# Kernel tuning notes

Measured on AMD Instinct MI355X. Metric: run time of the kernel, lower is better.

The kernel has to match this reference:

```python
import jax, jax.numpy as jnp
import numpy as np

NV = 6890          # SMPL vertex count
NF = 13776         # SMPL face count
N_CHUNKS = 10
EUCL_THRES = 0.02  # euclthres
WN_THRES = 0.99    # exterior if winding number <= 0.99


def _winding_numbers(points, tris):
    """Generalized winding numbers of `points` [m,3] w.r.t. triangle soup `tris` [f,3,3].
    Solid angle per (point, triangle) via the van-Oosterom/Strackee atan2 formula."""
    r = tris[None, :, :, :] - points[:, None, None, :]   # [m,f,3,3]
    ra, rb, rc = r[:, :, 0, :], r[:, :, 1, :], r[:, :, 2, :]
    la = jnp.linalg.norm(ra, axis=-1)
    lb = jnp.linalg.norm(rb, axis=-1)
    lc = jnp.linalg.norm(rc, axis=-1)
    det = jnp.einsum('mfi,mfi->mf', ra, jnp.cross(rb, rc))
    denom = (la * lb * lc
             + jnp.sum(ra * rb, -1) * lc
             + jnp.sum(rb * rc, -1) * la
             + jnp.sum(rc * ra, -1) * lb)
    omega = 2.0 * jnp.arctan2(det, denom)                # [m,f]
    return jnp.sum(omega, axis=-1) / (4.0 * jnp.pi)      # [m]


def setup_inputs() -> dict:
    key = jax.random.key(0)
    k1, k2, k3 = jax.random.split(key, 3)
    vertices = jax.random.normal(k1, (1, NV, 3), dtype=jnp.float32)
    faces = jax.random.randint(k2, (NF, 3), 0, NV)
    # geodesic-distance >= geothres mask: symmetric, False on the diagonal
    gm = jax.random.uniform(k3, (NV, NV)) > 0.3
    gm = gm & gm.T
    gm = gm.at[jnp.arange(NV), jnp.arange(NV)].set(False)
    return {"vertices": vertices, "faces": faces, "geomask": gm}


def reference(vertices, faces, geomask):
    # triangles(vertices): gather face corner coordinates  [NF,3,3] (bs=1)
    tris = vertices[0][faces]
    # get_intersection_mask: chunked winding numbers, exterior = wn <= 0.99
    pts = vertices[0].reshape(N_CHUNKS, NV // N_CHUNKS, 3)
    wn = jax.lax.map(lambda p: _winding_numbers(p, tris), pts).reshape(NV)
    exterior = (wn <= WN_THRES)[None, :]                 # [1,NV] bool
    # batch_pairwise_dist (squared=False)
    x = vertices[0]                                      # [NV,3]
    sq = jnp.sum(x * x, axis=-1)
    d2 = sq[:, None] + sq[None, :] - 2.0 * (x @ x.T)
    v2v = jnp.sqrt(jnp.maximum(d2, 0.0))                 # [NV,NV]
    # mask geodesically-near pairs with inf, take per-vertex min over dim 1
    masked = jnp.where(geomask, v2v, jnp.inf)
    idx = jnp.argmin(masked, axis=0)                     # argmin over rows for each column
    v2v_min = v2v[jnp.arange(NV), idx][None, :]          # gather along dim 2 (symmetric)
    incontact = v2v_min < EUCL_THRES
    return v2v_min, incontact, exterior
```

## Files before the change

kernel.cpp:

```cpp
#include <hip/hip_runtime.h>
#include <hip/hip_bf16.h>
#include <math.h>

#define NV 6890
#define NF 13776
#define NVPAD 6912
#define NPBLK 27
#define TCH 64
#define TPC 216
#define WN_THRES 0.99
#define EUCL_THRES 0.02f

#define WS_TRIS_OFF   64
#define WS_X4_OFF     (64 + NF*48)
#define WS_PART_OFF   (64 + NF*48 + NV*16)

__global__ __launch_bounds__(256) void prep_kernel(
    const float* __restrict__ verts, const int* __restrict__ faces,
    const unsigned char* __restrict__ gm_bytes,
    float* __restrict__ tris12, float* __restrict__ x4, int* __restrict__ flag)
{
    int t = blockIdx.x * 256 + threadIdx.x;

    if (t < NF) {
        int ia = faces[t*3+0], ib = faces[t*3+1], ic = faces[t*3+2];
        float* o = tris12 + (size_t)t * 12;
        o[0]  = verts[ia*3+0]; o[1]  = verts[ia*3+1]; o[2]  = verts[ia*3+2]; o[3]  = 0.f;
        o[4]  = verts[ib*3+0]; o[5]  = verts[ib*3+1]; o[6]  = verts[ib*3+2]; o[7]  = 0.f;
        o[8]  = verts[ic*3+0]; o[9]  = verts[ic*3+1]; o[10] = verts[ic*3+2]; o[11] = 0.f;
    }
    if (t < NV) {
        float x = verts[t*3+0], y = verts[t*3+1], z = verts[t*3+2];
        x4[t*4+0] = x; x4[t*4+1] = y; x4[t*4+2] = z;
        x4[t*4+3] = (x*x + y*y) + z*z;
    }
    if (blockIdx.x == 0 && threadIdx.x < 64) {
        int lane = threadIdx.x;
        bool any3F = false, anyNZmod = false;
        for (int k = 0; k < 64; ++k) {
            int off = lane * 64 + k;
            unsigned char b = gm_bytes[off];
            if ((off & 3) == 3 && (b == 0x3F || b == 0xBF)) any3F = true;
            if ((off & 3) != 0 && b != 0) anyNZmod = true;
        }
        unsigned long long m3F = __ballot(any3F);
        unsigned long long mNZ = __ballot(anyNZmod);
        if (lane == 0) {
            *flag = m3F ? 2 : (mNZ ? 0 : 1);
        }
    }
}

__device__ __forceinline__ float fast_atan2f(float y, float x)
{
    float ay = __builtin_fabsf(y), ax = __builtin_fabsf(x);
    float mx = fmaxf(ax, ay);
    float mn = fminf(ax, ay);
    float r  = __builtin_amdgcn_rcpf(fmaxf(mx, 1e-37f));
    float t  = mn * r;
    float s  = t * t;
    float u  =              0.00282363896258175373077393f;
    u = fmaf(u, s, -0.0159569028764963150024414f);
    u = fmaf(u, s,  0.0425049886107444763183594f);
    u = fmaf(u, s, -0.0748900920152664184570312f);
    u = fmaf(u, s,  0.106347933411598205566406f);
    u = fmaf(u, s, -0.142027363181114196777344f);
    u = fmaf(u, s,  0.199926957488059997558594f);
    u = fmaf(u, s, -0.333331018686294555664062f);
    float p = fmaf(s * u, t, t);
    p = (ay > ax)  ? (1.5707963267948966f - p) : p;
    p = (x < 0.0f) ? (3.14159265358979323846f - p) : p;
    return copysignf(p, y);
}

__global__ __launch_bounds__(256) void wn_kernel(
    const float4* __restrict__ tris12, const float4* __restrict__ x4,
    float* __restrict__ partials)
{
    int pt = blockIdx.x * 256 + threadIdx.x;
    int tc = blockIdx.y;
    int t0 = tc * TPC;
    int nt = min(TPC, NF - t0);

    float4 P = x4[min(pt, NV - 1)];
    float px = P.x, py = P.y, pz = P.z;

    const float4* __restrict__ T = tris12 + (size_t)t0 * 3;

    double acc = 0.0;
    #pragma unroll 2
    for (int k = 0; k < nt; ++k) {
        float4 A = T[3*k+0];
        float4 B = T[3*k+1];
        float4 C = T[3*k+2];
        float ax = A.x - px, ay = A.y - py, az = A.z - pz;
        float bx = B.x - px, by = B.y - py, bz = B.z - pz;
        float cx = C.x - px, cy = C.y - py, cz = C.z - pz;

        float la = __builtin_amdgcn_sqrtf((ax*ax + ay*ay) + az*az);
        float lb = __builtin_amdgcn_sqrtf((bx*bx + by*by) + bz*bz);
        float lc = __builtin_amdgcn_sqrtf((cx*cx + cy*cy) + cz*cz);

        float ux = by*cz - bz*cy;
        float uy = bz*cx - bx*cz;
        float uz = bx*cy - by*cx;
        float det = (ax*ux + ay*uy) + az*uz;

        float dab = (ax*bx + ay*by) + az*bz;
        float dbc = (bx*cx + by*cy) + bz*cz;
        float dca = (cx*ax + cy*ay) + cz*az;

        float denom = la*lb*lc + dab*lc + dbc*la + dca*lb;

        acc += (double)fast_atan2f(det, denom);
    }

    partials[(size_t)tc * NVPAD + pt] = (float)acc;
}

__global__ __launch_bounds__(256) void wn_reduce_kernel(
    const float* __restrict__ partials, float* __restrict__ out_exterior)
{
    int pt = blockIdx.x * 256 + threadIdx.x;
    if (pt >= NV) return;
    double s = 0.0;
    for (int t = 0; t < TCH; ++t) s += (double)partials[(size_t)t * NVPAD + pt];
    double wn = (2.0 * s) / 12.566370614359172953850573533118;
    out_exterior[pt] = (wn <= WN_THRES) ? 1.0f : 0.0f;
}

__device__ __forceinline__ void acc_min(float& m, const float4* __restrict__ x4,
                                        int i, bool g,
                                        float xj, float yj, float zj, float sqj)
{
    float4 vi = x4[i];
    float dot = (vi.x*xj + vi.y*yj) + vi.z*zj;
    float d2  = vi.w + sqj - 2.0f * dot;
    m = fminf(m, g ? d2 : INFINITY);
}

__global__ __launch_bounds__(256) void v2v_kernel(
    const void* __restrict__ gm, const float4* __restrict__ x4,
    const int* __restrict__ flag_p, float* __restrict__ out)
{
    int j = blockIdx.x;
    int tid = threadIdx.x;
    int flag = *flag_p;

    float4 vj = x4[j];
    float xj = vj.x, yj = vj.y, zj = vj.z, sqj = vj.w;

    float m = INFINITY;

    if (flag == 0) {
        const unsigned char* row = (const unsigned char*)gm + (size_t)j * NV;
        int lead = (int)((4u - ((uintptr_t)row & 3u)) & 3u);
        int nw = (NV - lead) >> 2;
        int base = lead + nw * 4;
        int ntail = NV - base;
        if (tid < lead) acc_min(m, x4, tid, row[tid] != 0, xj, yj, zj, sqj);
        const unsigned int* wrow = (const unsigned int*)(row + lead);
        for (int w = tid; w < nw; w += 256) {
            unsigned int v = wrow[w];
            int i0 = lead + w * 4;
            acc_min(m, x4, i0+0, (v & 0x000000FFu) != 0, xj, yj, zj, sqj);
            acc_min(m, x4, i0+1, (v & 0x0000FF00u) != 0, xj, yj, zj, sqj);
            acc_min(m, x4, i0+2, (v & 0x00FF0000u) != 0, xj, yj, zj, sqj);
            acc_min(m, x4, i0+3, (v & 0xFF000000u) != 0, xj, yj, zj, sqj);
        }
        if (tid < ntail) acc_min(m, x4, base + tid, row[base + tid] != 0, xj, yj, zj, sqj);
    } else if (flag == 1) {
        const uint2* row = (const uint2*)((const int*)gm + (size_t)j * NV);
        for (int w = tid; w < NV/2; w += 256) {
            uint2 v = row[w];
            int i0 = w * 2;
            acc_min(m, x4, i0+0, v.x != 0, xj, yj, zj, sqj);
            acc_min(m, x4, i0+1, v.y != 0, xj, yj, zj, sqj);
        }
    } else {
        const float2* row = (const float2*)((const float*)gm + (size_t)j * NV);
        for (int w = tid; w < NV/2; w += 256) {
            float2 v = row[w];
            int i0 = w * 2;
            acc_min(m, x4, i0+0, v.x != 0.0f, xj, yj, zj, sqj);
            acc_min(m, x4, i0+1, v.y != 0.0f, xj, yj, zj, sqj);
        }
    }

    __shared__ float red[256];
    red[tid] = m;
    __syncthreads();
    for (int s = 128; s > 0; s >>= 1) {
        if (tid < s) red[tid] = fminf(red[tid], red[tid + s]);
        __syncthreads();
    }
    if (tid == 0) {
        float d = __builtin_amdgcn_sqrtf(fmaxf(red[0], 0.f));
        out[j] = d;
        out[NV + j] = (d < EUCL_THRES) ? 1.f : 0.f;
    }
}

extern "C" void kernel_launch(void* const* d_in, const int* in_sizes, int n_in,
                              void* d_out, int out_size, void* d_ws, size_t ws_size,
                              hipStream_t stream)
{
    const float* verts = (const float*)d_in[0];
    const int*   faces = (const int*)d_in[1];
    const void*  gm    = d_in[2];
    float* out = (float*)d_out;
    char* ws = (char*)d_ws;

    int*   flag     = (int*)ws;
    float* tris12   = (float*)(ws + WS_TRIS_OFF);
    float* x4       = (float*)(ws + WS_X4_OFF);
    float* partials = (float*)(ws + WS_PART_OFF);

    int nprep = (NF > NV ? NF : NV);
    prep_kernel<<<(nprep + 255) / 256, 256, 0, stream>>>(
        verts, faces, (const unsigned char*)gm, tris12, x4, flag);

    wn_kernel<<<dim3(NPBLK, TCH), 256, 0, stream>>>(
        (const float4*)tris12, (const float4*)x4, partials);

    wn_reduce_kernel<<<NPBLK, 256, 0, stream>>>(partials, out + 2 * NV);

    v2v_kernel<<<NV, 256, 0, stream>>>(gm, (const float4*)x4, flag, out);
}
```

Baseline: 520.9 us.

## Fuse v2v and winding-number kernels into one launch with wave-per-row v2v

Merges the pairwise-distance min kernel and the winding-number kernel into a single launch, with blocks split by index between the two jobs so both run concurrently. The v2v path now gives each 64-lane wave one row and reduces with shuffles instead of a shared-memory tree with block barriers. The triangle and point buffers are padded with zeros so the winding loop runs a fixed trip count with 4-way unrolling, and each group of four atan2 results is summed in float before being added to the double accumulator. Risks include byte-wise gm loads that are no longer vectorized, a slight precision change from float partial sums, and load imbalance between the two block types.

New measurement: 501.9 us. 3.7% less time.

```diff
diff --git a/kernel.cpp b/kernel.cpp
--- a/kernel.cpp
+++ b/kernel.cpp
@@ -1,19 +1,21 @@
 #include <hip/hip_runtime.h>
-#include <hip/hip_bf16.h>
 #include <math.h>
 
 #define NV 6890
 #define NF 13776
 #define NVPAD 6912
+#define NFPAD 13824
 #define NPBLK 27
 #define TCH 64
 #define TPC 216
+#define V2V_BLOCKS 1723
+#define WN_BLOCKS (NPBLK*TCH)
 #define WN_THRES 0.99
 #define EUCL_THRES 0.02f
 
 #define WS_TRIS_OFF   64
-#define WS_X4_OFF     (64 + NF*48)
-#define WS_PART_OFF   (64 + NF*48 + NV*16)
+#define WS_X4_OFF     (64 + NFPAD*48)
+#define WS_PART_OFF   (WS_X4_OFF + NVPAD*16)
 
 __global__ __launch_bounds__(256) void prep_kernel(
     const float* __restrict__ verts, const int* __restrict__ faces,
@@ -22,17 +24,26 @@
 {
     int t = blockIdx.x * 256 + threadIdx.x;
 
-    if (t < NF) {
-        int ia = faces[t*3+0], ib = faces[t*3+1], ic = faces[t*3+2];
+    if (t < NFPAD) {
         float* o = tris12 + (size_t)t * 12;
-        o[0]  = verts[ia*3+0]; o[1]  = verts[ia*3+1]; o[2]  = verts[ia*3+2]; o[3]  = 0.f;
-        o[4]  = verts[ib*3+0]; o[5]  = verts[ib*3+1]; o[6]  = verts[ib*3+2]; o[7]  = 0.f;
-        o[8]  = verts[ic*3+0]; o[9]  = verts[ic*3+1]; o[10] = verts[ic*3+2]; o[11] = 0.f;
-    }
-    if (t < NV) {
-        float x = verts[t*3+0], y = verts[t*3+1], z = verts[t*3+2];
-        x4[t*4+0] = x; x4[t*4+1] = y; x4[t*4+2] = z;
-        x4[t*4+3] = (x*x + y*y) + z*z;
+        if (t < NF) {
+            int ia = faces[t*3+0], ib = faces[t*3+1], ic = faces[t*3+2];
+            o[0]  = verts[ia*3+0]; o[1]  = verts[ia*3+1]; o[2]  = verts[ia*3+2]; o[3]  = 0.f;
+            o[4]  = verts[ib*3+0]; o[5]  = verts[ib*3+1]; o[6]  = verts[ib*3+2]; o[7]  = 0.f;
+            o[8]  = verts[ic*3+0]; o[9]  = verts[ic*3+1]; o[10] = verts[ic*3+2]; o[11] = 0.f;
+        } else {
+            #pragma unroll
+            for (int q = 0; q < 12; ++q) o[q] = 0.f;
+        }
+    }
+    if (t < NVPAD) {
+        if (t < NV) {
+            float x = verts[t*3+0], y = verts[t*3+1], z = verts[t*3+2];
+            x4[t*4+0] = x; x4[t*4+1] = y; x4[t*4+2] = z;
+            x4[t*4+3] = (x*x + y*y) + z*z;
+        } else {
+            x4[t*4+0] = 0.f; x4[t*4+1] = 0.f; x4[t*4+2] = 0.f; x4[t*4+3] = 0.f;
+        }
     }
     if (blockIdx.x == 0 && threadIdx.x < 64) {
         int lane = threadIdx.x;
@@ -73,49 +84,108 @@
     return copysignf(p, y);
 }
 
-__global__ __launch_bounds__(256) void wn_kernel(
+__global__ __launch_bounds__(256) void fused_kernel(
     const float4* __restrict__ tris12, const float4* __restrict__ x4,
-    float* __restrict__ partials)
-{
-    int pt = blockIdx.x * 256 + threadIdx.x;
-    int tc = blockIdx.y;
-    int t0 = tc * TPC;
-    int nt = min(TPC, NF - t0);
-
-    float4 P = x4[min(pt, NV - 1)];
-    float px = P.x, py = P.y, pz = P.z;
-
-    const float4* __restrict__ T = tris12 + (size_t)t0 * 3;
-
-    double acc = 0.0;
-    #pragma unroll 2
-    for (int k = 0; k < nt; ++k) {
-        float4 A = T[3*k+0];
-        float4 B = T[3*k+1];
-        float4 C = T[3*k+2];
-        float ax = A.x - px, ay = A.y - py, az = A.z - pz;
-        float bx = B.x - px, by = B.y - py, bz = B.z - pz;
-        float cx = C.x - px, cy = C.y - py, cz = C.z - pz;
-
-        float la = __builtin_amdgcn_sqrtf((ax*ax + ay*ay) + az*az);
-        float lb = __builtin_amdgcn_sqrtf((bx*bx + by*by) + bz*bz);
-        float lc = __builtin_amdgcn_sqrtf((cx*cx + cy*cy) + cz*cz);
-
-        float ux = by*cz - bz*cy;
-        float uy = bz*cx - bx*cz;
-        float uz = bx*cy - by*cx;
-        float det = (ax*ux + ay*uy) + az*uz;
-
-        float dab = (ax*bx + ay*by) + az*bz;
-        float dbc = (bx*cx + by*cy) + bz*cz;
-        float dca = (cx*ax + cy*ay) + cz*az;
-
-        float denom = la*lb*lc + dab*lc + dbc*la + dca*lb;
-
-        acc += (double)fast_atan2f(det, denom);
-    }
-
-    partials[(size_t)tc * NVPAD + pt] = (float)acc;
+    float* __restrict__ partials,
+    const void* __restrict__ gm, const int* __restrict__ flag_p,
+    float* __restrict__ out)
+{
+    if (blockIdx.x < V2V_BLOCKS) {
+        int w = threadIdx.x >> 6;
+        int lane = threadIdx.x & 63;
+        int j = blockIdx.x * 4 + w;
+        if (j >= NV) return;
+
+        int flag = *flag_p;
+        float4 vj = x4[j];
+        float m = INFINITY;
+
+#define V2V_BODY(GTEST)                                            \
+        {                                                          \
+            int i0 = 0;                                            \
+            for (; i0 + 64 <= NV; i0 += 64) {                      \
+                int i = i0 + lane;                                 \
+                bool g = (GTEST);                                  \
+                float4 vi = x4[i];                                 \
+                float dot = (vi.x*vj.x + vi.y*vj.y) + vi.z*vj.z;   \
+                float d2  = vi.w + vj.w - 2.0f*dot;                \
+                m = fminf(m, g ? d2 : INFINITY);                   \
+            }                                                      \
+            int i = i0 + lane;                                     \
+            if (i < NV) {                                          \
+                bool g = (GTEST);                                  \
+                float4 vi = x4[i];                                 \
+                float dot = (vi.x*vj.x + vi.y*vj.y) + vi.z*vj.z;   \
+                float d2  = vi.w + vj.w - 2.0f*dot;                \
+                m = fminf(m, g ? d2 : INFINITY);                   \
+            }                                                      \
+        }
+
+        if (flag == 0) {
+            const unsigned char* row = (const unsigned char*)gm + (size_t)j * NV;
+            V2V_BODY(row[i] != 0)
+        } else if (flag == 1) {
+            const int* row = (const int*)gm + (size_t)j * NV;
+            V2V_BODY(row[i] != 0)
+        } else {
+            const float* row = (const float*)gm + (size_t)j * NV;
+            V2V_BODY(row[i] != 0.0f)
+        }
+#undef V2V_BODY
+
+        #pragma unroll
+        for (int k = 32; k > 0; k >>= 1)
+            m = fminf(m, __shfl_xor(m, k, 64));
+        if (lane == 0) {
+            float d = __builtin_amdgcn_sqrtf(fmaxf(m, 0.f));
+            out[j] = d;
+            out[NV + j] = (d < EUCL_THRES) ? 1.f : 0.f;
+        }
+    } else {
+        int wnb = blockIdx.x - V2V_BLOCKS;
+        int tc = wnb / NPBLK;
+        int pb = wnb - tc * NPBLK;
+        int pt = pb * 256 + threadIdx.x;
+
+        float4 P = x4[pt];
+        float px = P.x, py = P.y, pz = P.z;
+        const float4* __restrict__ T = tris12 + (size_t)tc * (TPC * 3);
+
+        double acc = 0.0;
+        for (int kk = 0; kk < TPC; kk += 4) {
+            float s4 = 0.f;
+            #pragma unroll
+            for (int u = 0; u < 4; ++u) {
+                const float4* Tk = T + 3 * (kk + u);
+                float4 A = Tk[0];
+                float4 B = Tk[1];
+                float4 C = Tk[2];
+                float ax = A.x - px, ay = A.y - py, az = A.z - pz;
+                float bx = B.x - px, by = B.y - py, bz = B.z - pz;
+                float cx = C.x - px, cy = C.y - py, cz = C.z - pz;
+
+                float la = __builtin_amdgcn_sqrtf((ax*ax + ay*ay) + az*az);
+                float lb = __builtin_amdgcn_sqrtf((bx*bx + by*by) + bz*bz);
+                float lc = __builtin_amdgcn_sqrtf((cx*cx + cy*cy) + cz*cz);
+
+                float ux = by*cz - bz*cy;
+                float uy = bz*cx - bx*cz;
+                float uz = bx*cy - by*cx;
+                float det = (ax*ux + ay*uy) + az*uz;
+
+                float dab = (ax*bx + ay*by) + az*bz;
+                float dbc = (bx*cx + by*cy) + bz*cz;
+                float dca = (cx*ax + cy*ay) + cz*az;
+
+                float denom = la*lb*lc + dab*lc + dbc*la + dca*lb;
+
+                s4 += fast_atan2f(det, denom);
+            }
+            acc += (double)s4;
+        }
+
+        partials[(size_t)tc * NVPAD + pt] = (float)acc;
+    }
 }
 
 __global__ __launch_bounds__(256) void wn_reduce_kernel(
@@ -129,78 +199,6 @@
     out_exterior[pt] = (wn <= WN_THRES) ? 1.0f : 0.0f;
 }
 
-__device__ __forceinline__ void acc_min(float& m, const float4* __restrict__ x4,
-                                        int i, bool g,
-                                        float xj, float yj, float zj, float sqj)
-{
-    float4 vi = x4[i];
-    float dot = (vi.x*xj + vi.y*yj) + vi.z*zj;
-    float d2  = vi.w + sqj - 2.0f * dot;
-    m = fminf(m, g ? d2 : INFINITY);
-}
-
-__global__ __launch_bounds__(256) void v2v_kernel(
-    const void* __restrict__ gm, const float4* __restrict__ x4,
-    const int* __restrict__ flag_p, float* __restrict__ out)
-{
-    int j = blockIdx.x;
-    int tid = threadIdx.x;
-    int flag = *flag_p;
-
-    float4 vj = x4[j];
-    float xj = vj.x, yj = vj.y, zj = vj.z, sqj = vj.w;
-
-    float m = INFINITY;
-
-    if (flag == 0) {
-        const unsigned char* row = (const unsigned char*)gm + (size_t)j * NV;
-        int lead = (int)((4u - ((uintptr_t)row & 3u)) & 3u);
-        int nw = (NV - lead) >> 2;
-        int base = lead + nw * 4;
-        int ntail = NV - base;
-        if (tid < lead) acc_min(m, x4, tid, row[tid] != 0, xj, yj, zj, sqj);
-        const unsigned int* wrow = (const unsigned int*)(row + lead);
-        for (int w = tid; w < nw; w += 256) {
-            unsigned int v = wrow[w];
-            int i0 = lead + w * 4;
-            acc_min(m, x4, i0+0, (v & 0x000000FFu) != 0, xj, yj, zj, sqj);
-            acc_min(m, x4, i0+1, (v & 0x0000FF00u) != 0, xj, yj, zj, sqj);
-            acc_min(m, x4, i0+2, (v & 0x00FF0000u) != 0, xj, yj, zj, sqj);
-            acc_min(m, x4, i0+3, (v & 0xFF000000u) != 0, xj, yj, zj, sqj);
-        }
-        if (tid < ntail) acc_min(m, x4, base + tid, row[base + tid] != 0, xj, yj, zj, sqj);
-    } else if (flag == 1) {
-        const uint2* row = (const uint2*)((const int*)gm + (size_t)j * NV);
-        for (int w = tid; w < NV/2; w += 256) {
-            uint2 v = row[w];
-            int i0 = w * 2;
-            acc_min(m, x4, i0+0, v.x != 0, xj, yj, zj, sqj);
-            acc_min(m, x4, i0+1, v.y != 0, xj, yj, zj, sqj);
-        }
-    } else {
-        const float2* row = (const float2*)((const float*)gm + (size_t)j * NV);
-        for (int w = tid; w < NV/2; w += 256) {
-            float2 v = row[w];
-            int i0 = w * 2;
-            acc_min(m, x4, i0+0, v.x != 0.0f, xj, yj, zj, sqj);
-            acc_min(m, x4, i0+1, v.y != 0.0f, xj, yj, zj, sqj);
-        }
-    }
-
-    __shared__ float red[256];
-    red[tid] = m;
-    __syncthreads();
-    for (int s = 128; s > 0; s >>= 1) {
-        if (tid < s) red[tid] = fminf(red[tid], red[tid + s]);
-        __syncthreads();
-    }
-    if (tid == 0) {
-        float d = __builtin_amdgcn_sqrtf(fmaxf(red[0], 0.f));
-        out[j] = d;
-        out[NV + j] = (d < EUCL_THRES) ? 1.f : 0.f;
-    }
-}
-
 extern "C" void kernel_launch(void* const* d_in, const int* in_sizes, int n_in,
                               void* d_out, int out_size, void* d_ws, size_t ws_size,
                               hipStream_t stream)
@@ -216,14 +214,11 @@
     float* x4       = (float*)(ws + WS_X4_OFF);
     float* partials = (float*)(ws + WS_PART_OFF);
 
-    int nprep = (NF > NV ? NF : NV);
-    prep_kernel<<<(nprep + 255) / 256, 256, 0, stream>>>(
+    prep_kernel<<<NFPAD / 256, 256, 0, stream>>>(
         verts, faces, (const unsigned char*)gm, tris12, x4, flag);
 
-    wn_kernel<<<dim3(NPBLK, TCH), 256, 0, stream>>>(
-        (const float4*)tris12, (const float4*)x4, partials);
+    fused_kernel<<<V2V_BLOCKS + WN_BLOCKS, 256, 0, stream>>>(
+        (const float4*)tris12, (const float4*)x4, partials, gm, flag, out);
 
     wn_reduce_kernel<<<NPBLK, 256, 0, stream>>>(partials, out + 2 * NV);
-
-    v2v_kernel<<<NV, 256, 0, stream>>>(gm, (const float4*)x4, flag, out);
-}
+}
```
